# Performance work log

Measured on AMD Instinct MI355X. Metric: run time of the kernel, lower is better.

The kernel has to match this reference:

```python
import jax, jax.numpy as jnp
import numpy as np

D_MODEL = 1024
N_HEADS = 16
HEAD_DIM = D_MODEL // N_HEADS
D_FF = 4096
EPS = 1e-5


def _layer_norm(x, gamma, beta):
    mu = jnp.mean(x, axis=-1, keepdims=True)
    var = jnp.var(x, axis=-1, keepdims=True)
    return (x - mu) * jax.lax.rsqrt(var + EPS) * gamma + beta


def setup_inputs() -> dict:
    key = jax.random.key(0)
    ks = jax.random.split(key, 16)
    B, T, S = 2, 2048, 2048
    s = 1.0 / np.sqrt(D_MODEL)
    inp = {
        "tgt": jax.random.normal(ks[0], (B, T, D_MODEL), jnp.float32),
        "memory": jax.random.normal(ks[1], (B, S, D_MODEL), jnp.float32),
        "wq": jax.random.normal(ks[2], (D_MODEL, D_MODEL), jnp.float32) * s,
        "bq": jnp.zeros((D_MODEL,), jnp.float32),
        "wk": jax.random.normal(ks[3], (D_MODEL, D_MODEL), jnp.float32) * s,
        "bk": jnp.zeros((D_MODEL,), jnp.float32),
        "wv": jax.random.normal(ks[4], (D_MODEL, D_MODEL), jnp.float32) * s,
        "bv": jnp.zeros((D_MODEL,), jnp.float32),
        "wo": jax.random.normal(ks[5], (D_MODEL, D_MODEL), jnp.float32) * s,
        "bo": jnp.zeros((D_MODEL,), jnp.float32),
        "w1": jax.random.normal(ks[6], (D_MODEL, D_FF), jnp.float32) * s,
        "b1": jnp.zeros((D_FF,), jnp.float32),
        "w2": jax.random.normal(ks[7], (D_FF, D_MODEL), jnp.float32) * (1.0 / np.sqrt(D_FF)),
        "b2": jnp.zeros((D_MODEL,), jnp.float32),
        "g1": jnp.ones((D_MODEL,), jnp.float32),
        "be1": jnp.zeros((D_MODEL,), jnp.float32),
        "g2": jnp.ones((D_MODEL,), jnp.float32),
        "be2": jnp.zeros((D_MODEL,), jnp.float32),
    }
    return inp


def reference(tgt, memory, wq, bq, wk, bk, wv, bv, wo, bo, w1, b1, w2, b2, g1, be1, g2, be2):
    B, T, _ = tgt.shape
    S = memory.shape[1]
    scale = HEAD_DIM ** -0.5
    # projections -> [B, H, L, Dh]
    Q = (tgt @ wq + bq).reshape(B, T, N_HEADS, HEAD_DIM).transpose(0, 2, 1, 3)
    K = (memory @ wk + bk).reshape(B, S, N_HEADS, HEAD_DIM).transpose(0, 2, 1, 3)
    V = (memory @ wv + bv).reshape(B, S, N_HEADS, HEAD_DIM).transpose(0, 2, 1, 3)
    scores = jnp.einsum("bhtd,bhsd->bhts", Q, K) * scale
    attn = jax.nn.softmax(scores, axis=-1)  # dropout=0 (eval)
    ctx = jnp.einsum("bhts,bhsd->bhtd", attn, V)
    ctx = ctx.transpose(0, 2, 1, 3).reshape(B, T, D_MODEL)
    attn_out = ctx @ wo + bo
    # post-norm residual blocks
    x = _layer_norm(tgt + attn_out, g1, be1)
    ff = jax.nn.relu(x @ w1 + b1) @ w2 + b2
    out = _layer_norm(x + ff, g2, be2)
    return out
```

## Files before the change

### kernel.cpp

```cpp
#include <hip/hip_runtime.h>


typedef unsigned short u16;
typedef __attribute__((ext_vector_type(8))) short bvec8;
typedef __attribute__((ext_vector_type(4))) float fvec4;

#define MFMA16(a, b, c) __builtin_amdgcn_mfma_f32_16x16x32_bf16((a), (b), (c), 0, 0, 0)

__device__ __forceinline__ u16 f2b(float f) {
  union { float f; unsigned u; } x; x.f = f;
  unsigned u = x.u;
  return (u16)((u + 0x7FFFu + ((u >> 16) & 1u)) >> 16);
}
__device__ __forceinline__ u16 f2b_t(float f) {
  union { float f; unsigned u; } x; x.f = f;
  return (u16)(x.u >> 16);
}
__device__ __forceinline__ void gl_lds16(const u16* g, u16* lds) {
  __builtin_amdgcn_global_load_lds(
      (const __attribute__((address_space(1))) void*)g,
      (__attribute__((address_space(3))) void*)lds, 16, 0, 0);
}

__global__ __launch_bounds__(256) void k_pre(
    const float* __restrict__ tgt, const float* __restrict__ mem,
    const float* __restrict__ wq, const float* __restrict__ wk,
    const float* __restrict__ wv, const float* __restrict__ wo,
    const float* __restrict__ w1, const float* __restrict__ w2,
    u16* __restrict__ tgt_b, u16* __restrict__ mem_b,
    u16* __restrict__ wqT, u16* __restrict__ wkvT, u16* __restrict__ woT,
    u16* __restrict__ w1T, u16* __restrict__ w2T) {
  __shared__ float t[32][33];
  int bb = blockIdx.x;
  if (bb < 8192) {
    const float* in = (bb < 4096) ? tgt : mem;
    u16* outp = (bb < 4096) ? tgt_b : mem_b;
    int i = (bb & 4095) * 256 + threadIdx.x;
    float4 v = ((const float4*)in)[i];
    ushort4 o;
    o.x = f2b(v.x); o.y = f2b(v.y); o.z = f2b(v.z); o.w = f2b(v.w);
    ((ushort4*)outp)[i] = o;
    return;
  }
  int b = bb - 8192;
  const float* W; u16* WT; int K, N, bx, by;
  if (b < 4096) {
    int m = b >> 10, tt = b & 1023;
    bx = tt & 31; by = tt >> 5; K = 1024; N = 1024;
    W = (m == 0) ? wq : (m == 1) ? wk : (m == 2) ? wv : wo;
    WT = (m == 0) ? wqT : (m == 1) ? wkvT : (m == 2) ? wkvT + 1024 * 1024 : woT;
  } else if (b < 8192) {
    int tt = b - 4096; bx = tt & 127; by = tt >> 7; K = 1024; N = 4096;
    W = w1; WT = w1T;
  } else {
    int tt = b - 8192; bx = tt & 31; by = tt >> 5; K = 4096; N = 1024;
    W = w2; WT = w2T;
  }
  int tx = threadIdx.x & 31, ty = threadIdx.x >> 5;
  int n0 = bx * 32, k0 = by * 32;
#pragma unroll
  for (int i = 0; i < 4; i++)
    t[ty + i * 8][tx] = W[(size_t)(k0 + ty + i * 8) * N + n0 + tx];
  __syncthreads();
#pragma unroll
  for (int i = 0; i < 4; i++)
    WT[(size_t)(n0 + ty + i * 8) * K + k0 + tx] = f2b(t[tx][ty + i * 8]);
}

__global__ __launch_bounds__(256, 3) void k_qkv(
    const u16* __restrict__ tgt_b, const u16* __restrict__ mem_b,
    const u16* __restrict__ wqT, const u16* __restrict__ wkvT,
    const float* __restrict__ bq, const float* __restrict__ bk,
    const float* __restrict__ bv,
    u16* __restrict__ Qb, u16* __restrict__ Kb, u16* __restrict__ Vtb) {
  __shared__ u16 S[256 * 32];
  const int tid = threadIdx.x, w = tid >> 6, lane = tid & 63;
  const int q = lane >> 4, l = lane & 15;
  const bool isQ = blockIdx.x < 256;
  const int id = isQ ? blockIdx.x : blockIdx.x - 256;
  const int nx = isQ ? 8 : 16;
  const int m0 = (id / nx) * 128, n0 = (id % nx) * 128;
  const u16* A = isQ ? tgt_b : mem_b;
  const u16* BT = isQ ? wqT : wkvT;
  const int wm = (w >> 1) * 64, wn = (w & 1) * 64;
  const int srow = lane >> 2, sgrp = lane & 3;
  const int gcol = ((sgrp + (srow >> 1)) & 3) * 8;
  const int rpos = ((q + 4 - ((l >> 1) & 3)) & 3) * 8;
  const u16* gp[4];
  u16* lp[4];
#pragma unroll
  for (int c = 0; c < 4; c++) {
    int r0 = (w * 4 + c) * 16;
    gp[c] = (r0 < 128) ? A + (size_t)(m0 + r0 + srow) * 1024 + gcol
                       : BT + (size_t)(n0 + r0 - 128 + srow) * 1024 + gcol;
    lp[c] = &S[r0 * 32];
  }
  fvec4 acc[4][4] = {};
#pragma unroll 1
  for (int k0 = 0; k0 < 1024; k0 += 32) {
#pragma unroll
    for (int c = 0; c < 4; c++) gl_lds16(gp[c] + k0, lp[c]);
    __syncthreads();
    bvec8 af[4], bf[4];
#pragma unroll
    for (int i = 0; i < 4; i++) {
      af[i] = *(const bvec8*)&S[(wm + 16 * i + l) * 32 + rpos];
      bf[i] = *(const bvec8*)&S[(128 + wn + 16 * i + l) * 32 + rpos];
    }
#pragma unroll
    for (int i = 0; i < 4; i++)
#pragma unroll
      for (int j = 0; j < 4; j++)
        acc[i][j] = MFMA16(af[i], bf[j], acc[i][j]);
    __syncthreads();
  }
#pragma unroll
  for (int mi = 0; mi < 4; mi++)
#pragma unroll
    for (int ni = 0; ni < 4; ni++) {
      int row = m0 + wm + mi * 16 + q * 4;
      int col = n0 + wn + ni * 16 + l;
      if (isQ) {
        float bvv = bq[col];
#pragma unroll
        for (int r = 0; r < 4; r++)
          Qb[(size_t)(row + r) * 1024 + col] = f2b((acc[mi][ni][r] + bvv) * 0.125f);
      } else if (col < 1024) {
        float bvv = bk[col];
#pragma unroll
        for (int r = 0; r < 4; r++)
          Kb[(size_t)(row + r) * 1024 + col] = f2b(acc[mi][ni][r] + bvv);
      } else {
        int vcol = col - 1024;
        float bvv = bv[vcol];
        int b = row >> 11, s = row & 2047;
        int h = vcol >> 6, d = vcol & 63;
        ushort4 o;
        o.x = f2b(acc[mi][ni][0] + bvv);
        o.y = f2b(acc[mi][ni][1] + bvv);
        o.z = f2b(acc[mi][ni][2] + bvv);
        o.w = f2b(acc[mi][ni][3] + bvv);
        *(ushort4*)&Vtb[((size_t)(b * 16 + h) * 64 + d) * 2048 + s] = o;
      }
    }
}

template <int TM, int TN>
__global__ __launch_bounds__(256, TM == 64 ? 4 : 3) void k_gemm(
    const u16* __restrict__ A, const u16* __restrict__ BT,
    const float* __restrict__ bias, const float* __restrict__ resid,
    float* __restrict__ outF, u16* __restrict__ outB,
    int M, int N, int Kstride, int Klen, float scale, int flags) {
  constexpr int WM = TM / 2, WN = TN / 2;
  constexpr int MI = WM / 16, NI = WN / 16;
  constexpr int NCALL = (TM + TN) / 64;
  __shared__ u16 S[(TM + TN) * 32];
  const int tid = threadIdx.x, w = tid >> 6, lane = tid & 63;
  const int q = lane >> 4, l = lane & 15;
  const int m0 = blockIdx.y * TM, n0 = blockIdx.x * TN;
  const int kbeg = blockIdx.z * Klen;
  const int wm = (w >> 1) * WM, wn = (w & 1) * WN;
  const int srow = lane >> 2, sgrp = lane & 3;
  const int gcol = ((sgrp + (srow >> 1)) & 3) * 8;
  const int rpos = ((q + 4 - ((l >> 1) & 3)) & 3) * 8;
  const u16* gp[NCALL];
  u16* lp[NCALL];
#pragma unroll
  for (int c = 0; c < NCALL; c++) {
    int r0 = (w * NCALL + c) * 16;
    gp[c] = (r0 < TM) ? A + (size_t)(m0 + r0 + srow) * Kstride + kbeg + gcol
                      : BT + (size_t)(n0 + r0 - TM + srow) * Kstride + kbeg + gcol;
    lp[c] = &S[r0 * 32];
  }
  fvec4 acc[MI][NI] = {};
#pragma unroll 1
  for (int k0 = 0; k0 < Klen; k0 += 32) {
#pragma unroll
    for (int c = 0; c < NCALL; c++) gl_lds16(gp[c] + k0, lp[c]);
    __syncthreads();
    bvec8 af[MI], bf[NI];
#pragma unroll
    for (int i = 0; i < MI; i++)
      af[i] = *(const bvec8*)&S[(wm + 16 * i + l) * 32 + rpos];
#pragma unroll
    for (int j = 0; j < NI; j++)
      bf[j] = *(const bvec8*)&S[(TM + wn + 16 * j + l) * 32 + rpos];
#pragma unroll
    for (int i = 0; i < MI; i++)
#pragma unroll
      for (int j = 0; j < NI; j++)
        acc[i][j] = MFMA16(af[i], bf[j], acc[i][j]);
    __syncthreads();
  }
  if (flags & 16) {
    float* po = outF + (size_t)blockIdx.z * M * N;
#pragma unroll
    for (int mi = 0; mi < MI; mi++)
#pragma unroll
      for (int ni = 0; ni < NI; ni++) {
        int row = m0 + wm + mi * 16 + q * 4;
        int col = n0 + wn + ni * 16 + l;
#pragma unroll
        for (int r = 0; r < 4; r++)
          po[(size_t)(row + r) * N + col] = acc[mi][ni][r];
      }
    return;
  }
#pragma unroll
  for (int mi = 0; mi < MI; mi++)
#pragma unroll
    for (int ni = 0; ni < NI; ni++) {
      int row = m0 + wm + mi * 16 + q * 4;
      int col = n0 + wn + ni * 16 + l;
      float bvv = bias[col];
#pragma unroll
      for (int r = 0; r < 4; r++) {
        float v = (acc[mi][ni][r] + bvv) * scale;
        if (flags & 1) v = fmaxf(v, 0.0f);
        size_t idx = (size_t)(row + r) * N + col;
        if (flags & 8) v += resid[idx];
        if (flags & 2) outB[idx] = f2b(v);
        if (flags & 4) outF[idx] = v;
      }
    }
}

__global__ __launch_bounds__(256, 4) void k_attn(
    const u16* __restrict__ Q, const u16* __restrict__ Kb,
    const u16* __restrict__ Vt, float* __restrict__ opart,
    float* __restrict__ lpart) {
  __shared__ u16 Ks[64 * 64];
  __shared__ u16 Vs[64 * 64];
  __shared__ u16 Ps[4][2][16 * 72];
  const int tid = threadIdx.x, w = tid >> 6, lane = tid & 63;
  const int q = lane >> 4, l = lane & 15;
  const int blk = blockIdx.x;
  const int bh = blk >> 4, tb = blk & 15;
  const int b = bh >> 4, h = bh & 15;
  const int t0 = tb * 128 + w * 32;
  const int sbeg = blockIdx.y * 1024;
  float* op = opart + (size_t)blockIdx.y * 4096 * 1024;
  float* lp = lpart + (size_t)blockIdx.y * 4096 * 16;
  const u16* Qp = Q + (size_t)(b * 2048 + t0) * 1024 + h * 64;
  const u16* Kp = Kb + (size_t)(b * 2048) * 1024 + h * 64;
  const u16* Vp = Vt + (size_t)bh * 64 * 2048;
  const int rowin = lane >> 3, grp = lane & 7;
  const int gcol = ((grp + rowin) & 7) * 8;
  const int kc0 = ((q + 8 - (l & 7)) & 7) * 8;
  const int kc1 = ((q + 12 - (l & 7)) & 7) * 8;
  bvec8 aQ[2][2];
#pragma unroll
  for (int ti = 0; ti < 2; ti++)
#pragma unroll
    for (int kh = 0; kh < 2; kh++)
      aQ[ti][kh] = *(const bvec8*)&Qp[(size_t)(ti * 16 + l) * 1024 + kh * 32 + q * 8];
  fvec4 o[2][4] = {};
  float ls[2][4] = {};
#pragma unroll 1
  for (int s0 = sbeg; s0 < sbeg + 1024; s0 += 64) {
    gl_lds16(Kp + (size_t)(s0 + w * 8 + rowin) * 1024 + gcol, &Ks[(w * 8) * 64]);
    gl_lds16(Kp + (size_t)(s0 + 32 + w * 8 + rowin) * 1024 + gcol, &Ks[(32 + w * 8) * 64]);
    gl_lds16(Vp + (size_t)(w * 8 + rowin) * 2048 + s0 + gcol, &Vs[(w * 8) * 64]);
    gl_lds16(Vp + (size_t)(32 + w * 8 + rowin) * 2048 + s0 + gcol, &Vs[(32 + w * 8) * 64]);
    __syncthreads();
    fvec4 sc[2][4];
#pragma unroll
    for (int ti = 0; ti < 2; ti++)
#pragma unroll
      for (int ss = 0; ss < 4; ss++) sc[ti][ss] = (fvec4){0.f, 0.f, 0.f, 0.f};
#pragma unroll
    for (int ss = 0; ss < 4; ss++) {
      const int ro = (ss * 16 + l) * 64;
      bvec8 kf0 = *(const bvec8*)&Ks[ro + kc0];
      bvec8 kf1 = *(const bvec8*)&Ks[ro + kc1];
#pragma unroll
      for (int ti = 0; ti < 2; ti++) {
        sc[ti][ss] = MFMA16(aQ[ti][0], kf0, sc[ti][ss]);
        sc[ti][ss] = MFMA16(aQ[ti][1], kf1, sc[ti][ss]);
      }
    }
#pragma unroll
    for (int ti = 0; ti < 2; ti++)
#pragma unroll
      for (int ss = 0; ss < 4; ss++)
#pragma unroll
        for (int r = 0; r < 4; r++) {
          float p = __expf(sc[ti][ss][r]);
          ls[ti][r] += p;
          Ps[w][ti][(q * 4 + r) * 72 + ss * 16 + l] = f2b_t(p);
        }
    asm volatile("s_waitcnt lgkmcnt(0)" ::: "memory");
    bvec8 bV[4][2];
#pragma unroll
    for (int dt = 0; dt < 4; dt++) {
      const int ro = (dt * 16 + l) * 64;
      bV[dt][0] = *(const bvec8*)&Vs[ro + kc0];
      bV[dt][1] = *(const bvec8*)&Vs[ro + kc1];
    }
#pragma unroll
    for (int ti = 0; ti < 2; ti++) {
      bvec8 aP0 = *(const bvec8*)&Ps[w][ti][l * 72 + q * 8];
      bvec8 aP1 = *(const bvec8*)&Ps[w][ti][l * 72 + 32 + q * 8];
#pragma unroll
      for (int dt = 0; dt < 4; dt++) {
        o[ti][dt] = MFMA16(aP0, bV[dt][0], o[ti][dt]);
        o[ti][dt] = MFMA16(aP1, bV[dt][1], o[ti][dt]);
      }
    }
    __syncthreads();
  }
#pragma unroll
  for (int ti = 0; ti < 2; ti++)
#pragma unroll
    for (int r = 0; r < 4; r++) {
      float s = ls[ti][r];
      s += __shfl_xor(s, 1, 64);
      s += __shfl_xor(s, 2, 64);
      s += __shfl_xor(s, 4, 64);
      s += __shfl_xor(s, 8, 64);
      int trow = b * 2048 + t0 + ti * 16 + q * 4 + r;
      if (l == 0) lp[trow * 16 + h] = s;
#pragma unroll
      for (int dt = 0; dt < 4; dt++)
        op[(size_t)trow * 1024 + h * 64 + dt * 16 + l] = o[ti][dt][r];
    }
}

__global__ __launch_bounds__(256) void k_actx(const float* __restrict__ opart,
                                              const float* __restrict__ lpart,
                                              u16* __restrict__ ctx) {
  int row = blockIdx.x, c0 = threadIdx.x * 4;
  int h = c0 >> 6;
  float lsum = lpart[row * 16 + h] + lpart[4096 * 16 + row * 16 + h];
  float inv = 1.0f / lsum;
  float4 a = *(const float4*)&opart[(size_t)row * 1024 + c0];
  float4 b = *(const float4*)&opart[(size_t)4096 * 1024 + (size_t)row * 1024 + c0];
  ushort4 o;
  o.x = f2b((a.x + b.x) * inv);
  o.y = f2b((a.y + b.y) * inv);
  o.z = f2b((a.z + b.z) * inv);
  o.w = f2b((a.w + b.w) * inv);
  *(ushort4*)&ctx[(size_t)row * 1024 + c0] = o;
}

__global__ __launch_bounds__(256) void k_lnp(
    const float* __restrict__ parts, int nparts,
    const float* __restrict__ bias, const float* __restrict__ resid,
    const float* __restrict__ g, const float* __restrict__ be,
    float* __restrict__ xf, u16* __restrict__ xb) {
  __shared__ float sm[8];
  int row = blockIdx.x, tid = threadIdx.x;
  size_t base = (size_t)row * 1024;
  const size_t pstride = (size_t)4096 * 1024;
  float v[4], s = 0.f, ss = 0.f;
#pragma unroll
  for (int j = 0; j < 4; j++) {
    int c = tid + j * 256;
    float acc = bias[c] + resid[base + c];
    for (int z = 0; z < nparts; z++) acc += parts[z * pstride + base + c];
    v[j] = acc;
    s += acc; ss += acc * acc;
  }
#pragma unroll
  for (int off = 32; off; off >>= 1) {
    s += __shfl_down(s, off, 64);
    ss += __shfl_down(ss, off, 64);
  }
  int w = tid >> 6;
  if ((tid & 63) == 0) { sm[w] = s; sm[4 + w] = ss; }
  __syncthreads();
  float S = sm[0] + sm[1] + sm[2] + sm[3];
  float SS = sm[4] + sm[5] + sm[6] + sm[7];
  float mean = S * (1.0f / 1024.0f);
  float var = SS * (1.0f / 1024.0f) - mean * mean;
  float rstd = rsqrtf(var + 1e-5f);
#pragma unroll
  for (int j = 0; j < 4; j++) {
    int c = tid + j * 256;
    float o = (v[j] - mean) * rstd * g[c] + be[c];
    xf[base + c] = o;
    if (xb) xb[base + c] = f2b(o);
  }
}

extern "C" void kernel_launch(void* const* d_in, const int* in_sizes, int n_in,
                              void* d_out, int out_size, void* d_ws, size_t ws_size,
                              hipStream_t stream) {
  (void)in_sizes; (void)n_in; (void)out_size; (void)ws_size;
  const float* tgt = (const float*)d_in[0];
  const float* mem = (const float*)d_in[1];
  const float* wq  = (const float*)d_in[2];
  const float* bq  = (const float*)d_in[3];
  const float* wk  = (const float*)d_in[4];
  const float* bk  = (const float*)d_in[5];
  const float* wv  = (const float*)d_in[6];
  const float* bv  = (const float*)d_in[7];
  const float* wo  = (const float*)d_in[8];
  const float* bo  = (const float*)d_in[9];
  const float* w1  = (const float*)d_in[10];
  const float* b1  = (const float*)d_in[11];
  const float* w2  = (const float*)d_in[12];
  const float* b2  = (const float*)d_in[13];
  const float* g1  = (const float*)d_in[14];
  const float* be1 = (const float*)d_in[15];
  const float* g2  = (const float*)d_in[16];
  const float* be2 = (const float*)d_in[17];
  float* out = (float*)d_out;

  char* ws = (char*)d_ws;
  size_t off = 0;
  auto take = [&](size_t bytes) { char* p = ws + off; off += bytes; return p; };
  const size_t MB = 1024 * 1024;
  u16* tgt_b = (u16*)take(8 * MB);
  u16* mem_b = (u16*)take(8 * MB);
  u16* wqT   = (u16*)take(2 * MB);
  u16* wkvT  = (u16*)take(4 * MB);
  u16* woT   = (u16*)take(2 * MB);
  u16* w1T   = (u16*)take(8 * MB);
  u16* w2T   = (u16*)take(8 * MB);
  u16* Qb    = (u16*)take(8 * MB);
  u16* Kb    = (u16*)take(8 * MB);
  u16* Vtb   = (u16*)take(8 * MB);
  u16* ctx   = (u16*)take(8 * MB);
  float* opart = (float*)take(32 * MB);
  float* opj   = (float*)take(32 * MB);
  float* lpart = (float*)take(1 * MB);
  float* xf  = (float*)take(16 * MB);
  u16* xb    = (u16*)take(8 * MB);
  u16* hbuf  = Qb;
  float* fp2 = opart;

  k_pre<<<20480, 256, 0, stream>>>(tgt, mem, wq, wk, wv, wo, w1, w2,
                                   tgt_b, mem_b, wqT, wkvT, woT, w1T, w2T);
  k_qkv<<<768, 256, 0, stream>>>(tgt_b, mem_b, wqT, wkvT, bq, bk, bv,
                                 Qb, Kb, Vtb);
  k_attn<<<dim3(512, 2), 256, 0, stream>>>(Qb, Kb, Vtb, opart, lpart);
  k_actx<<<4096, 256, 0, stream>>>(opart, lpart, ctx);
  k_gemm<64, 128><<<dim3(8, 64, 2), 256, 0, stream>>>(
      ctx, woT, nullptr, nullptr, opj, nullptr,
      4096, 1024, 1024, 512, 1.0f, 16);
  k_lnp<<<4096, 256, 0, stream>>>(opj, 2, bo, tgt, g1, be1, xf, xb);
  k_gemm<128, 128><<<dim3(32, 32), 256, 0, stream>>>(
      xb, w1T, b1, nullptr, nullptr, hbuf,
      4096, 4096, 1024, 1024, 1.0f, 1 | 2);
  k_gemm<64, 128><<<dim3(8, 64, 2), 256, 0, stream>>>(
      hbuf, w2T, nullptr, nullptr, fp2, nullptr,
      4096, 1024, 4096, 2048, 1.0f, 16);
  k_lnp<<<4096, 256, 0, stream>>>(fp2, 2, b2, xf, g2, be2, out, nullptr);
}
```

Measured before the change: 403.8 us.

## Double K-step to 64 with 8-way LDS swizzle; drop split-K for out-proj

The QKV and generic GEMM kernels now stage a 64-wide K slice per iteration instead of 32. Each slice is loaded with 8 rows per 16-byte load group and a new 8-way XOR-style swizzle, then consumed in two MFMA half-steps. This halves the barrier and loop overhead per unit of K and raises the occupancy hint to 4 blocks per CU. The output-projection GEMM also drops its 2-way split-K, so the following layernorm reads one partial instead of two. That cuts fp32 partial traffic but halves the grid for that GEMM. The cost is doubled LDS per block, which may limit residency.

```diff
diff --git a/kernel.cpp b/kernel.cpp
--- a/kernel.cpp
+++ b/kernel.cpp
@@ -67,13 +67,13 @@
     WT[(size_t)(n0 + ty + i * 8) * K + k0 + tx] = f2b(t[tx][ty + i * 8]);
 }
 
-__global__ __launch_bounds__(256, 3) void k_qkv(
+__global__ __launch_bounds__(256, 4) void k_qkv(
     const u16* __restrict__ tgt_b, const u16* __restrict__ mem_b,
     const u16* __restrict__ wqT, const u16* __restrict__ wkvT,
     const float* __restrict__ bq, const float* __restrict__ bk,
     const float* __restrict__ bv,
     u16* __restrict__ Qb, u16* __restrict__ Kb, u16* __restrict__ Vtb) {
-  __shared__ u16 S[256 * 32];
+  __shared__ u16 S[256 * 64];
   const int tid = threadIdx.x, w = tid >> 6, lane = tid & 63;
   const int q = lane >> 4, l = lane & 15;
   const bool isQ = blockIdx.x < 256;
@@ -83,35 +83,40 @@
   const u16* A = isQ ? tgt_b : mem_b;
   const u16* BT = isQ ? wqT : wkvT;
   const int wm = (w >> 1) * 64, wn = (w & 1) * 64;
-  const int srow = lane >> 2, sgrp = lane & 3;
-  const int gcol = ((sgrp + (srow >> 1)) & 3) * 8;
-  const int rpos = ((q + 4 - ((l >> 1) & 3)) & 3) * 8;
-  const u16* gp[4];
-  u16* lp[4];
-#pragma unroll
-  for (int c = 0; c < 4; c++) {
-    int r0 = (w * 4 + c) * 16;
-    gp[c] = (r0 < 128) ? A + (size_t)(m0 + r0 + srow) * 1024 + gcol
-                       : BT + (size_t)(n0 + r0 - 128 + srow) * 1024 + gcol;
-    lp[c] = &S[r0 * 32];
+  const int rowin = lane >> 3, grp = lane & 7;
+  const int gcol = ((grp + rowin) & 7) * 8;
+  const int kc0 = ((q + 8 - (l & 7)) & 7) * 8;
+  const int kc1 = ((q + 12 - (l & 7)) & 7) * 8;
+  const u16* gp[8];
+  u16* lp[8];
+#pragma unroll
+  for (int c = 0; c < 8; c++) {
+    int r0 = (w * 8 + c) * 8;
+    gp[c] = (r0 < 128) ? A + (size_t)(m0 + r0 + rowin) * 1024 + gcol
+                       : BT + (size_t)(n0 + r0 - 128 + rowin) * 1024 + gcol;
+    lp[c] = &S[r0 * 64];
   }
   fvec4 acc[4][4] = {};
 #pragma unroll 1
-  for (int k0 = 0; k0 < 1024; k0 += 32) {
-#pragma unroll
-    for (int c = 0; c < 4; c++) gl_lds16(gp[c] + k0, lp[c]);
-    __syncthreads();
-    bvec8 af[4], bf[4];
-#pragma unroll
-    for (int i = 0; i < 4; i++) {
-      af[i] = *(const bvec8*)&S[(wm + 16 * i + l) * 32 + rpos];
-      bf[i] = *(const bvec8*)&S[(128 + wn + 16 * i + l) * 32 + rpos];
-    }
-#pragma unroll
-    for (int i = 0; i < 4; i++)
-#pragma unroll
-      for (int j = 0; j < 4; j++)
-        acc[i][j] = MFMA16(af[i], bf[j], acc[i][j]);
+  for (int k0 = 0; k0 < 1024; k0 += 64) {
+#pragma unroll
+    for (int c = 0; c < 8; c++) gl_lds16(gp[c] + k0, lp[c]);
+    __syncthreads();
+#pragma unroll
+    for (int kh = 0; kh < 2; kh++) {
+      const int kc = kh ? kc1 : kc0;
+      bvec8 af[4], bf[4];
+#pragma unroll
+      for (int i = 0; i < 4; i++) {
+        af[i] = *(const bvec8*)&S[(wm + 16 * i + l) * 64 + kc];
+        bf[i] = *(const bvec8*)&S[(128 + wn + 16 * i + l) * 64 + kc];
+      }
+#pragma unroll
+      for (int i = 0; i < 4; i++)
+#pragma unroll
+        for (int j = 0; j < 4; j++)
+          acc[i][j] = MFMA16(af[i], bf[j], acc[i][j]);
+    }
     __syncthreads();
   }
 #pragma unroll
@@ -146,50 +151,55 @@
 }
 
 template <int TM, int TN>
-__global__ __launch_bounds__(256, TM == 64 ? 4 : 3) void k_gemm(
+__global__ __launch_bounds__(256, 4) void k_gemm(
     const u16* __restrict__ A, const u16* __restrict__ BT,
     const float* __restrict__ bias, const float* __restrict__ resid,
     float* __restrict__ outF, u16* __restrict__ outB,
     int M, int N, int Kstride, int Klen, float scale, int flags) {
   constexpr int WM = TM / 2, WN = TN / 2;
   constexpr int MI = WM / 16, NI = WN / 16;
-  constexpr int NCALL = (TM + TN) / 64;
-  __shared__ u16 S[(TM + TN) * 32];
+  constexpr int NCALL = (TM + TN) / 32;
+  __shared__ u16 S[(TM + TN) * 64];
   const int tid = threadIdx.x, w = tid >> 6, lane = tid & 63;
   const int q = lane >> 4, l = lane & 15;
   const int m0 = blockIdx.y * TM, n0 = blockIdx.x * TN;
   const int kbeg = blockIdx.z * Klen;
   const int wm = (w >> 1) * WM, wn = (w & 1) * WN;
-  const int srow = lane >> 2, sgrp = lane & 3;
-  const int gcol = ((sgrp + (srow >> 1)) & 3) * 8;
-  const int rpos = ((q + 4 - ((l >> 1) & 3)) & 3) * 8;
+  const int rowin = lane >> 3, grp = lane & 7;
+  const int gcol = ((grp + rowin) & 7) * 8;
+  const int kc0 = ((q + 8 - (l & 7)) & 7) * 8;
+  const int kc1 = ((q + 12 - (l & 7)) & 7) * 8;
   const u16* gp[NCALL];
   u16* lp[NCALL];
 #pragma unroll
   for (int c = 0; c < NCALL; c++) {
-    int r0 = (w * NCALL + c) * 16;
-    gp[c] = (r0 < TM) ? A + (size_t)(m0 + r0 + srow) * Kstride + kbeg + gcol
-                      : BT + (size_t)(n0 + r0 - TM + srow) * Kstride + kbeg + gcol;
-    lp[c] = &S[r0 * 32];
+    int r0 = (w * NCALL + c) * 8;
+    gp[c] = (r0 < TM) ? A + (size_t)(m0 + r0 + rowin) * Kstride + kbeg + gcol
+                      : BT + (size_t)(n0 + r0 - TM + rowin) * Kstride + kbeg + gcol;
+    lp[c] = &S[r0 * 64];
   }
   fvec4 acc[MI][NI] = {};
 #pragma unroll 1
-  for (int k0 = 0; k0 < Klen; k0 += 32) {
+  for (int k0 = 0; k0 < Klen; k0 += 64) {
 #pragma unroll
     for (int c = 0; c < NCALL; c++) gl_lds16(gp[c] + k0, lp[c]);
     __syncthreads();
-    bvec8 af[MI], bf[NI];
-#pragma unroll
-    for (int i = 0; i < MI; i++)
-      af[i] = *(const bvec8*)&S[(wm + 16 * i + l) * 32 + rpos];
-#pragma unroll
-    for (int j = 0; j < NI; j++)
-      bf[j] = *(const bvec8*)&S[(TM + wn + 16 * j + l) * 32 + rpos];
-#pragma unroll
-    for (int i = 0; i < MI; i++)
+#pragma unroll
+    for (int kh = 0; kh < 2; kh++) {
+      const int kc = kh ? kc1 : kc0;
+      bvec8 af[MI], bf[NI];
+#pragma unroll
+      for (int i = 0; i < MI; i++)
+        af[i] = *(const bvec8*)&S[(wm + 16 * i + l) * 64 + kc];
 #pragma unroll
       for (int j = 0; j < NI; j++)
-        acc[i][j] = MFMA16(af[i], bf[j], acc[i][j]);
+        bf[j] = *(const bvec8*)&S[(TM + wn + 16 * j + l) * 64 + kc];
+#pragma unroll
+      for (int i = 0; i < MI; i++)
+#pragma unroll
+        for (int j = 0; j < NI; j++)
+          acc[i][j] = MFMA16(af[i], bf[j], acc[i][j]);
+    }
     __syncthreads();
   }
   if (flags & 16) {
@@ -436,10 +446,10 @@
                                  Qb, Kb, Vtb);
   k_attn<<<dim3(512, 2), 256, 0, stream>>>(Qb, Kb, Vtb, opart, lpart);
   k_actx<<<4096, 256, 0, stream>>>(opart, lpart, ctx);
-  k_gemm<64, 128><<<dim3(8, 64, 2), 256, 0, stream>>>(
+  k_gemm<64, 128><<<dim3(8, 64, 1), 256, 0, stream>>>(
       ctx, woT, nullptr, nullptr, opj, nullptr,
-      4096, 1024, 1024, 512, 1.0f, 16);
-  k_lnp<<<4096, 256, 0, stream>>>(opj, 2, bo, tgt, g1, be1, xf, xb);
+      4096, 1024, 1024, 1024, 1.0f, 16);
+  k_lnp<<<4096, 256, 0, stream>>>(opj, 1, bo, tgt, g1, be1, xf, xb);
   k_gemm<128, 128><<<dim3(32, 32), 256, 0, stream>>>(
       xb, w1T, b1, nullptr, nullptr, hbuf,
       4096, 4096, 1024, 1024, 1.0f, 1 | 2);
```

New measurement: 394.0 us. -2.4%, faster.
